# Kernel optimization log

Measured on AMD Instinct MI355X. Metric: run time of the kernel, lower is better.

## Reference

```python
import jax, jax.numpy as jnp
import numpy as np

WS = 16        # window size
NH = 8         # num heads
EPS = 1e-6
BN_EPS = 1e-5


def _l2norm(t):
    # normalize along the channel (d) axis, which is axis=-2, per position
    return t / jnp.linalg.norm(t, axis=-2, keepdims=True)


def setup_inputs() -> dict:
    key = jax.random.key(0)
    k1, k2, k3 = jax.random.split(key, 3)
    B, C, H, W = 8, 96, 256, 256
    x = jax.random.normal(k1, (B, C, H, W), dtype=jnp.float32)
    w_qkv = jax.random.normal(k2, (3 * C, C), dtype=jnp.float32) * (1.0 / np.sqrt(C))
    w_proj = jax.random.normal(k3, (C, C), dtype=jnp.float32) * (1.0 / np.sqrt(C))
    gamma = jnp.ones((C,), dtype=jnp.float32)
    beta = jnp.zeros((C,), dtype=jnp.float32)
    return {"x": x, "w_qkv": w_qkv, "w_proj": w_proj, "gamma": gamma, "beta": beta}


def reference(x, w_qkv, w_proj, gamma, beta):
    B, C, H, W = x.shape
    ws, nh = WS, NH
    d = C // nh
    # pad H, W up to multiples of ws (static shapes -> jit-safe)
    Hp = (H + ws - 1) // ws * ws
    Wp = (W + ws - 1) // ws * ws
    if (Hp, Wp) != (H, W):
        x = jnp.pad(x, ((0, 0), (0, 0), (0, Hp - H), (0, Wp - W)))
    hh, ww = Hp // ws, Wp // ws

    # 1x1 conv qkv projection (no bias)
    qkv = jnp.einsum('oc,bchw->bohw', w_qkv, x)  # [B, 3C, Hp, Wp]
    # rearrange 'b (qkv h d) (hh ws1) (ww ws2) -> qkv (b hh ww) h d (ws1 ws2)'
    qkv = qkv.reshape(B, 3, nh, d, hh, ws, ww, ws)
    qkv = qkv.transpose(1, 0, 4, 6, 2, 3, 5, 7).reshape(3, B * hh * ww, nh, d, ws * ws)
    q, k, v = qkv[0], qkv[1], qkv[2]  # each [bw, h, d, n]  (n = ws*ws)

    q = _l2norm(q).transpose(0, 1, 3, 2)  # [bw, h, n, d]
    k = _l2norm(k)                        # [bw, h, d, n]

    ksum = k.sum(axis=-1) + EPS           # [bw, h, d]
    tailor = 1.0 / (ws * ws + jnp.einsum('bhnc,bhc->bhn', q, ksum))  # [bw, h, n]

    kv = jnp.einsum('bhmn,bhcn->bhmc', k, v)     # [bw, h, d, d]
    attn = jnp.einsum('bhnm,bhmc->bhcn', q, kv)  # [bw, h, d, n]
    attn = attn + v.sum(axis=-1, keepdims=True)  # broadcast sum_n v over n
    attn = attn * tailor[:, :, None, :]

    # rearrange '(b hh ww) h d (ws1 ws2) -> b (h d) (hh ws1) (ww ws2)'
    out = attn.reshape(B, hh, ww, nh, d, ws, ws)
    out = out.transpose(0, 3, 4, 1, 5, 2, 6).reshape(B, C, Hp, Wp)
    out = out[:, :, :H, :W]

    # proj: 1x1 conv + BatchNorm2d (training-mode batch statistics)
    y = jnp.einsum('oc,bchw->bohw', w_proj, out)
    mean = y.mean(axis=(0, 2, 3), keepdims=True)
    var = y.var(axis=(0, 2, 3), keepdims=True)
    y = (y - mean) * jax.lax.rsqrt(var + BN_EPS)
    y = y * gamma[None, :, None, None] + beta[None, :, None, None]
    return y
```

## Files before the change

### kernel.cpp

```cpp
#include <hip/hip_runtime.h>

typedef short s8v __attribute__((ext_vector_type(8)));
typedef float f4v __attribute__((ext_vector_type(4)));

union F8 { int4 i; s8v s; };

__device__ __forceinline__ short f2bf(float f){
  union {float f; unsigned u;} v; v.f = f;
  unsigned r = (v.u + 0x7FFFu + ((v.u >> 16) & 1u)) >> 16;
  return (short)r;
}

#define MFMA(a,b,c) __builtin_amdgcn_mfma_f32_16x16x32_bf16((a),(b),(c),0,0,0)

#define WS_W2_OFF   58368
#define WS_ST_OFF   76800
#define WS_OUT_OFF  (1u<<20)

__global__ void prep_kernel(const float* __restrict__ wqkv, const float* __restrict__ wproj,
                            unsigned short* __restrict__ w1, unsigned short* __restrict__ w2,
                            float* __restrict__ stats){
  int i = blockIdx.x * 256 + threadIdx.x;
  for (int j = i; j < 304*96; j += gridDim.x * 256){
    int row = j / 96, c = j - row * 96;
    float v = (row < 288) ? wqkv[row * 96 + c] : 0.f;
    w1[j] = (unsigned short)f2bf(v);
  }
  for (int j = i; j < 96*96; j += gridDim.x * 256)
    w2[j] = (unsigned short)f2bf(wproj[j]);
  if (i < 192) stats[i] = 0.f;
}

__global__ __launch_bounds__(256) void attn_kernel(const float* __restrict__ x,
                                                   const unsigned short* __restrict__ w1,
                                                   float* __restrict__ outp){
  __shared__ short ks[16*264];
  __shared__ short vs[16*264];
  __shared__ short qsT[256*32];
  __shared__ short kvT[16*32];

  const int tid  = threadIdx.x;
  const int lane = tid & 63, wave = tid >> 6;
  const int quad = lane >> 4, col = lane & 15;
  const int wx = blockIdx.x, wy = blockIdx.y, b = blockIdx.z;
  const int h0 = wy * 16, w0 = wx * 16;

  for (int i = tid; i < 4*264; i += 256){
    int r = i / 264; int cc = i - r * 264; r += 12;
    short v = (r == 15) ? (short)0x3F80 : (short)0;
    ks[r*264 + cc] = v; vs[r*264 + cc] = v;
  }
  for (int i = tid; i < 256*32; i += 256){
    int m = i & 31;
    qsT[i] = (m == 12) ? (short)0x3F80 : (short)0;
  }
  for (int i = tid; i < 16*32; i += 256) kvT[i] = 0;

  const float* xb = x + ((size_t)b * 96 << 16);
  s8v Bf[4][3];
  #pragma unroll
  for (int jt = 0; jt < 4; ++jt){
    int t0 = wave * 64 + jt * 16;
    const float* px = xb + (size_t)(h0 + (t0 >> 4)) * 256 + (w0 + col);
    #pragma unroll
    for (int kt = 0; kt < 3; ++kt){
      F8 f;
      #pragma unroll
      for (int j = 0; j < 8; ++j){
        int c = kt * 32 + quad * 8 + j;
        f.s[j] = f2bf(px[(size_t)c << 16]);
      }
      Bf[jt][kt] = f.s;
    }
  }

  for (int h = 0; h < 8; ++h){
    s8v Af[3][3];
    #pragma unroll
    for (int mi = 0; mi < 3; ++mi){
      int row = mi * 96 + h * 12 + col;
      const unsigned short* pw = w1 + row * 96 + quad * 8;
      #pragma unroll
      for (int kt = 0; kt < 3; ++kt){
        F8 f; f.i = *(const int4*)(pw + kt * 32);
        Af[mi][kt] = f.s;
      }
    }
    f4v acc[3][4];
    #pragma unroll
    for (int mi = 0; mi < 3; ++mi)
      #pragma unroll
      for (int jt = 0; jt < 4; ++jt){
        f4v a = {0.f, 0.f, 0.f, 0.f};
        #pragma unroll
        for (int kt = 0; kt < 3; ++kt) a = MFMA(Af[mi][kt], Bf[jt][kt], a);
        acc[mi][jt] = a;
      }

    #pragma unroll
    for (int jt = 0; jt < 4; ++jt){
      int t = wave * 64 + jt * 16 + col;
      {
        f4v q = acc[0][jt];
        float s = (quad < 3) ? (q[0]*q[0] + q[1]*q[1] + q[2]*q[2] + q[3]*q[3]) : 0.f;
        s += __shfl_xor(s, 16, 64); s += __shfl_xor(s, 32, 64);
        float rq = rsqrtf(s);
        if (quad < 3){
          short4 pk; pk.x = f2bf(q[0]*rq); pk.y = f2bf(q[1]*rq); pk.z = f2bf(q[2]*rq); pk.w = f2bf(q[3]*rq);
          *(short4*)&qsT[t * 32 + quad * 4] = pk;
        }
      }
      {
        f4v k = acc[1][jt];
        float s = (quad < 3) ? (k[0]*k[0] + k[1]*k[1] + k[2]*k[2] + k[3]*k[3]) : 0.f;
        s += __shfl_xor(s, 16, 64); s += __shfl_xor(s, 32, 64);
        float rk = rsqrtf(s);
        f4v vv = acc[2][jt];
        if (quad < 3){
          #pragma unroll
          for (int r = 0; r < 4; ++r){
            ks[(quad*4 + r) * 264 + t] = f2bf(k[r] * rk);
            vs[(quad*4 + r) * 264 + t] = f2bf(vv[r]);
          }
        }
      }
    }
    __syncthreads();

    if (wave == 0){
      f4v kv = {0.f, 0.f, 0.f, 0.f};
      #pragma unroll
      for (int kk = 0; kk < 8; ++kk){
        F8 a, bb;
        a.i  = *(const int4*)&ks[col * 264 + kk * 32 + quad * 8];
        bb.i = *(const int4*)&vs[col * 264 + kk * 32 + quad * 8];
        kv = MFMA(a.s, bb.s, kv);
      }
      int c = col;
      if (c != 12){
        int row = (c == 15) ? 12 : c;
        if (quad < 3){
          short4 pk; pk.x = f2bf(kv[0]); pk.y = f2bf(kv[1]); pk.z = f2bf(kv[2]); pk.w = f2bf(kv[3]);
          *(short4*)&kvT[row * 32 + quad * 4] = pk;
        } else {
          short4 pk; pk.x = (c == 15) ? (short)0 : f2bf(kv[3]); pk.y = 0; pk.z = 0; pk.w = 0;
          *(short4*)&kvT[row * 32 + 12] = pk;
        }
      }
    }
    __syncthreads();

    {
      F8 af; af.i = *(const int4*)&kvT[col * 32 + quad * 8];
      #pragma unroll
      for (int jt = 0; jt < 4; ++jt){
        int t0 = wave * 64 + jt * 16;
        F8 bq; bq.i = *(const int4*)&qsT[(t0 + col) * 32 + quad * 8];
        f4v z = {0.f, 0.f, 0.f, 0.f};
        f4v d2 = MFMA(af.s, bq.s, z);
        float dot = __shfl(d2[0], 48 + col, 64);
        float tl = 1.f / (256.f + dot);
        if (quad < 3){
          float* po = outp + ((size_t)(b * 96 + h * 12 + quad * 4) << 16)
                      + (size_t)(h0 + (t0 >> 4)) * 256 + (w0 + col);
          #pragma unroll
          for (int r = 0; r < 4; ++r) po[(size_t)r << 16] = d2[r] * tl;
        }
      }
    }
    __syncthreads();
  }
}

__global__ __launch_bounds__(256) void proj_kernel(const float* __restrict__ outp,
                                                   const unsigned short* __restrict__ w2,
                                                   float* __restrict__ y,
                                                   float* __restrict__ stats){
  __shared__ float sld[192];
  const int tid = threadIdx.x;
  if (tid < 192) sld[tid] = 0.f;
  __syncthreads();
  const int lane = tid & 63, wave = tid >> 6;
  const int quad = lane >> 4, col = lane & 15;
  const int hrow = blockIdx.x, b = blockIdx.y;

  const float* ob = outp + ((size_t)b * 96 << 16) + (size_t)hrow * 256;
  s8v Bf[4][3];
  #pragma unroll
  for (int jt = 0; jt < 4; ++jt){
    int n0 = wave * 64 + jt * 16;
    const float* px = ob + n0 + col;
    #pragma unroll
    for (int kt = 0; kt < 3; ++kt){
      F8 f;
      #pragma unroll
      for (int j = 0; j < 8; ++j){
        int c = kt * 32 + quad * 8 + j;
        f.s[j] = f2bf(px[(size_t)c << 16]);
      }
      Bf[jt][kt] = f.s;
    }
  }
  float* yb = y + ((size_t)b * 96 << 16) + (size_t)hrow * 256;
  #pragma unroll
  for (int mt = 0; mt < 6; ++mt){
    s8v Af[3];
    #pragma unroll
    for (int kt = 0; kt < 3; ++kt){
      F8 f; f.i = *(const int4*)(w2 + (mt * 16 + col) * 96 + kt * 32 + quad * 8);
      Af[kt] = f.s;
    }
    float rs[4] = {0.f,0.f,0.f,0.f}, rss[4] = {0.f,0.f,0.f,0.f};
    #pragma unroll
    for (int jt = 0; jt < 4; ++jt){
      int n0 = wave * 64 + jt * 16;
      f4v a = {0.f, 0.f, 0.f, 0.f};
      #pragma unroll
      for (int kt = 0; kt < 3; ++kt) a = MFMA(Af[kt], Bf[jt][kt], a);
      float* pyo = yb + ((size_t)(mt * 16 + quad * 4) << 16) + n0 + col;
      #pragma unroll
      for (int r = 0; r < 4; ++r){
        float v = a[r];
        pyo[(size_t)r << 16] = v;
        rs[r] += v; rss[r] += v * v;
      }
    }
    #pragma unroll
    for (int r = 0; r < 4; ++r){
      float a1 = rs[r], a2 = rss[r];
      a1 += __shfl_xor(a1, 1, 64); a2 += __shfl_xor(a2, 1, 64);
      a1 += __shfl_xor(a1, 2, 64); a2 += __shfl_xor(a2, 2, 64);
      a1 += __shfl_xor(a1, 4, 64); a2 += __shfl_xor(a2, 4, 64);
      a1 += __shfl_xor(a1, 8, 64); a2 += __shfl_xor(a2, 8, 64);
      if (col == 0){
        int o = mt * 16 + quad * 4 + r;
        atomicAdd(&sld[o], a1);
        atomicAdd(&sld[96 + o], a2);
      }
    }
  }
  __syncthreads();
  if (tid < 192) atomicAdd(&stats[tid], sld[tid]);
}

__global__ __launch_bounds__(256) void bn_kernel(float* __restrict__ y,
                                                 const float* __restrict__ stats,
                                                 const float* __restrict__ gamma,
                                                 const float* __restrict__ beta){
  const int qq = blockIdx.x, c = blockIdx.y, b = blockIdx.z;
  const float invN = 1.f / 524288.f;
  float s = stats[c], ss = stats[96 + c];
  float mean = s * invN;
  float var  = ss * invN - mean * mean;
  float sc = gamma[c] * rsqrtf(var + 1e-5f);
  float sh = beta[c] - mean * sc;
  float4* p = (float4*)(y + ((size_t)(b * 96 + c) << 16) + (size_t)qq * 16384);
  int tid = threadIdx.x;
  #pragma unroll
  for (int i = 0; i < 16; ++i){
    float4 v = p[tid + i * 256];
    v.x = v.x * sc + sh; v.y = v.y * sc + sh; v.z = v.z * sc + sh; v.w = v.w * sc + sh;
    p[tid + i * 256] = v;
  }
}

extern "C" void kernel_launch(void* const* d_in, const int* in_sizes, int n_in,
                              void* d_out, int out_size, void* d_ws, size_t ws_size,
                              hipStream_t stream){
  const float* x     = (const float*)d_in[0];
  const float* wqkv  = (const float*)d_in[1];
  const float* wproj = (const float*)d_in[2];
  const float* gamma = (const float*)d_in[3];
  const float* beta  = (const float*)d_in[4];
  char* ws = (char*)d_ws;
  unsigned short* w1 = (unsigned short*)(ws);
  unsigned short* w2 = (unsigned short*)(ws + WS_W2_OFF);
  float* stats = (float*)(ws + WS_ST_OFF);
  float* outp  = (float*)(ws + WS_OUT_OFF);
  float* y = (float*)d_out;

  hipLaunchKernelGGL(prep_kernel, dim3(64), dim3(256), 0, stream, wqkv, wproj, w1, w2, stats);
  hipLaunchKernelGGL(attn_kernel, dim3(16, 16, 8), dim3(256), 0, stream, x, w1, outp);
  hipLaunchKernelGGL(proj_kernel, dim3(256, 8), dim3(256), 0, stream, outp, w2, y, stats);
  hipLaunchKernelGGL(bn_kernel, dim3(4, 96, 8), dim3(256), 0, stream, y, stats, gamma, beta);
}
```

Before: 613.4 us.

## Store attention output as bf16 channel-last and cut per-head syncs

The attention intermediate becomes bf16 in a pixel-major (channel-last) layout instead of fp32 channel-planar. This halves the intermediate traffic and lets the projection kernel load its operands as contiguous 16-byte vectors instead of strided scalar gathers plus conversion. The attention kernel double-buffers the k/v shared tiles and has every wave compute the kv product redundantly, building the transposed kv operand with lane shuffles, so two of the three barriers per head go away. The q, k and v projections are also computed one at a time to lower register pressure. The trade-offs are extra rounding on the intermediate, redundant MFMA work in every wave, and a tricky shuffle mapping that is easy to get wrong.

```diff
diff --git a/kernel.cpp b/kernel.cpp
--- a/kernel.cpp
+++ b/kernel.cpp
@@ -33,11 +33,10 @@
 
 __global__ __launch_bounds__(256) void attn_kernel(const float* __restrict__ x,
                                                    const unsigned short* __restrict__ w1,
-                                                   float* __restrict__ outp){
-  __shared__ short ks[16*264];
-  __shared__ short vs[16*264];
-  __shared__ short qsT[256*32];
-  __shared__ short kvT[16*32];
+                                                   short* __restrict__ outp){
+  __shared__ short ks[2][16*264];
+  __shared__ short vs[2][16*264];
+  __shared__ short qsT[256*40];
 
   const int tid  = threadIdx.x;
   const int lane = tid & 63, wave = tid >> 6;
@@ -45,16 +44,14 @@
   const int wx = blockIdx.x, wy = blockIdx.y, b = blockIdx.z;
   const int h0 = wy * 16, w0 = wx * 16;
 
-  for (int i = tid; i < 4*264; i += 256){
-    int r = i / 264; int cc = i - r * 264; r += 12;
+  for (int i = tid; i < 2*4*264; i += 256){
+    int buf = i / (4*264), j = i % (4*264);
+    int r = 12 + j / 264, cc = j % 264;
     short v = (r == 15) ? (short)0x3F80 : (short)0;
-    ks[r*264 + cc] = v; vs[r*264 + cc] = v;
-  }
-  for (int i = tid; i < 256*32; i += 256){
-    int m = i & 31;
-    qsT[i] = (m == 12) ? (short)0x3F80 : (short)0;
-  }
-  for (int i = tid; i < 16*32; i += 256) kvT[i] = 0;
+    ks[buf][r*264 + cc] = v; vs[buf][r*264 + cc] = v;
+  }
+  for (int i = tid; i < 256*40; i += 256)
+    qsT[i] = ((i % 40) == 12) ? (short)0x3F80 : (short)0;
 
   const float* xb = x + ((size_t)b * 96 << 16);
   s8v Bf[4][3];
@@ -75,104 +72,116 @@
   }
 
   for (int h = 0; h < 8; ++h){
-    s8v Af[3][3];
-    #pragma unroll
-    for (int mi = 0; mi < 3; ++mi){
-      int row = mi * 96 + h * 12 + col;
-      const unsigned short* pw = w1 + row * 96 + quad * 8;
+    const int p = h & 1;
+    {
+      s8v Aq[3];
       #pragma unroll
       for (int kt = 0; kt < 3; ++kt){
-        F8 f; f.i = *(const int4*)(pw + kt * 32);
-        Af[mi][kt] = f.s;
-      }
-    }
-    f4v acc[3][4];
-    #pragma unroll
-    for (int mi = 0; mi < 3; ++mi)
+        F8 f; f.i = *(const int4*)(w1 + (h*12 + col) * 96 + kt*32 + quad*8);
+        Aq[kt] = f.s;
+      }
       #pragma unroll
       for (int jt = 0; jt < 4; ++jt){
-        f4v a = {0.f, 0.f, 0.f, 0.f};
+        f4v a = {0.f,0.f,0.f,0.f};
         #pragma unroll
-        for (int kt = 0; kt < 3; ++kt) a = MFMA(Af[mi][kt], Bf[jt][kt], a);
-        acc[mi][jt] = a;
-      }
-
-    #pragma unroll
-    for (int jt = 0; jt < 4; ++jt){
-      int t = wave * 64 + jt * 16 + col;
-      {
-        f4v q = acc[0][jt];
-        float s = (quad < 3) ? (q[0]*q[0] + q[1]*q[1] + q[2]*q[2] + q[3]*q[3]) : 0.f;
+        for (int kt = 0; kt < 3; ++kt) a = MFMA(Aq[kt], Bf[jt][kt], a);
+        float s = (quad < 3) ? (a[0]*a[0] + a[1]*a[1] + a[2]*a[2] + a[3]*a[3]) : 0.f;
         s += __shfl_xor(s, 16, 64); s += __shfl_xor(s, 32, 64);
         float rq = rsqrtf(s);
         if (quad < 3){
-          short4 pk; pk.x = f2bf(q[0]*rq); pk.y = f2bf(q[1]*rq); pk.z = f2bf(q[2]*rq); pk.w = f2bf(q[3]*rq);
-          *(short4*)&qsT[t * 32 + quad * 4] = pk;
+          int t = wave*64 + jt*16 + col;
+          short4 pk; pk.x = f2bf(a[0]*rq); pk.y = f2bf(a[1]*rq); pk.z = f2bf(a[2]*rq); pk.w = f2bf(a[3]*rq);
+          *(short4*)&qsT[t*40 + quad*4] = pk;
         }
       }
-      {
-        f4v k = acc[1][jt];
-        float s = (quad < 3) ? (k[0]*k[0] + k[1]*k[1] + k[2]*k[2] + k[3]*k[3]) : 0.f;
+    }
+    {
+      s8v Ak[3];
+      #pragma unroll
+      for (int kt = 0; kt < 3; ++kt){
+        F8 f; f.i = *(const int4*)(w1 + (96 + h*12 + col) * 96 + kt*32 + quad*8);
+        Ak[kt] = f.s;
+      }
+      #pragma unroll
+      for (int jt = 0; jt < 4; ++jt){
+        f4v a = {0.f,0.f,0.f,0.f};
+        #pragma unroll
+        for (int kt = 0; kt < 3; ++kt) a = MFMA(Ak[kt], Bf[jt][kt], a);
+        float s = (quad < 3) ? (a[0]*a[0] + a[1]*a[1] + a[2]*a[2] + a[3]*a[3]) : 0.f;
         s += __shfl_xor(s, 16, 64); s += __shfl_xor(s, 32, 64);
         float rk = rsqrtf(s);
-        f4v vv = acc[2][jt];
         if (quad < 3){
+          int t = wave*64 + jt*16 + col;
           #pragma unroll
-          for (int r = 0; r < 4; ++r){
-            ks[(quad*4 + r) * 264 + t] = f2bf(k[r] * rk);
-            vs[(quad*4 + r) * 264 + t] = f2bf(vv[r]);
-          }
+          for (int r = 0; r < 4; ++r) ks[p][(quad*4 + r)*264 + t] = f2bf(a[r]*rk);
         }
       }
     }
+    {
+      s8v Av[3];
+      #pragma unroll
+      for (int kt = 0; kt < 3; ++kt){
+        F8 f; f.i = *(const int4*)(w1 + (192 + h*12 + col) * 96 + kt*32 + quad*8);
+        Av[kt] = f.s;
+      }
+      #pragma unroll
+      for (int jt = 0; jt < 4; ++jt){
+        f4v a = {0.f,0.f,0.f,0.f};
+        #pragma unroll
+        for (int kt = 0; kt < 3; ++kt) a = MFMA(Av[kt], Bf[jt][kt], a);
+        if (quad < 3){
+          int t = wave*64 + jt*16 + col;
+          #pragma unroll
+          for (int r = 0; r < 4; ++r) vs[p][(quad*4 + r)*264 + t] = f2bf(a[r]);
+        }
+      }
+    }
     __syncthreads();
 
-    if (wave == 0){
-      f4v kv = {0.f, 0.f, 0.f, 0.f};
-      #pragma unroll
-      for (int kk = 0; kk < 8; ++kk){
-        F8 a, bb;
-        a.i  = *(const int4*)&ks[col * 264 + kk * 32 + quad * 8];
-        bb.i = *(const int4*)&vs[col * 264 + kk * 32 + quad * 8];
-        kv = MFMA(a.s, bb.s, kv);
-      }
-      int c = col;
-      if (c != 12){
-        int row = (c == 15) ? 12 : c;
-        if (quad < 3){
-          short4 pk; pk.x = f2bf(kv[0]); pk.y = f2bf(kv[1]); pk.z = f2bf(kv[2]); pk.w = f2bf(kv[3]);
-          *(short4*)&kvT[row * 32 + quad * 4] = pk;
-        } else {
-          short4 pk; pk.x = (c == 15) ? (short)0 : f2bf(kv[3]); pk.y = 0; pk.z = 0; pk.w = 0;
-          *(short4*)&kvT[row * 32 + 12] = pk;
-        }
-      }
-    }
-    __syncthreads();
-
-    {
-      F8 af; af.i = *(const int4*)&kvT[col * 32 + quad * 8];
-      #pragma unroll
-      for (int jt = 0; jt < 4; ++jt){
-        int t0 = wave * 64 + jt * 16;
-        F8 bq; bq.i = *(const int4*)&qsT[(t0 + col) * 32 + quad * 8];
-        f4v z = {0.f, 0.f, 0.f, 0.f};
-        f4v d2 = MFMA(af.s, bq.s, z);
-        float dot = __shfl(d2[0], 48 + col, 64);
-        float tl = 1.f / (256.f + dot);
-        if (quad < 3){
-          float* po = outp + ((size_t)(b * 96 + h * 12 + quad * 4) << 16)
-                      + (size_t)(h0 + (t0 >> 4)) * 256 + (w0 + col);
-          #pragma unroll
-          for (int r = 0; r < 4; ++r) po[(size_t)r << 16] = d2[r] * tl;
-        }
-      }
-    }
-    __syncthreads();
-  }
-}
-
-__global__ __launch_bounds__(256) void proj_kernel(const float* __restrict__ outp,
+    f4v kvv = {0.f,0.f,0.f,0.f};
+    #pragma unroll
+    for (int kk = 0; kk < 8; ++kk){
+      F8 a, bv;
+      a.i  = *(const int4*)&ks[p][col*264 + kk*32 + quad*8];
+      bv.i = *(const int4*)&vs[p][col*264 + kk*32 + quad*8];
+      kvv = MFMA(a.s, bv.s, kvv);
+    }
+    F8 fa;
+    {
+      int cc = (col == 12) ? 15 : col;
+      int l0 = ((quad << 1) << 4) | cc;
+      int l1 = (((quad << 1) + 1) << 4) | cc;
+      float v;
+      v = __shfl(kvv[0], l0 & 63, 64); fa.s[0] = f2bf((quad < 2) ? v : 0.f);
+      v = __shfl(kvv[1], l0 & 63, 64); fa.s[1] = f2bf((quad < 2) ? v : 0.f);
+      v = __shfl(kvv[2], l0 & 63, 64); fa.s[2] = f2bf((quad < 2) ? v : 0.f);
+      v = __shfl(kvv[3], l0 & 63, 64); fa.s[3] = f2bf((quad < 2) ? v : 0.f);
+      float v0  = __shfl(kvv[0], l1 & 63, 64);
+      float v15 = __shfl(kvv[3], 48 | cc, 64);
+      fa.s[4] = f2bf((quad == 0) ? v0 : ((quad == 1) ? v15 : 0.f));
+      v = __shfl(kvv[1], l1 & 63, 64); fa.s[5] = f2bf((quad == 0) ? v : 0.f);
+      v = __shfl(kvv[2], l1 & 63, 64); fa.s[6] = f2bf((quad == 0) ? v : 0.f);
+      v = __shfl(kvv[3], l1 & 63, 64); fa.s[7] = f2bf((quad == 0) ? v : 0.f);
+    }
+    #pragma unroll
+    for (int jt = 0; jt < 4; ++jt){
+      int t0 = wave*64 + jt*16;
+      F8 bq; bq.i = *(const int4*)&qsT[(t0 + col)*40 + quad*8];
+      f4v z = {0.f,0.f,0.f,0.f};
+      f4v d2 = MFMA(fa.s, bq.s, z);
+      float dot = __shfl(d2[0], 48 + col, 64);
+      float tl = 1.f / dot;
+      if (quad < 3){
+        int pix = (h0 + (t0 >> 4)) * 256 + (w0 + col);
+        short* po = outp + ((size_t)(b << 16) + pix) * 96 + h*12 + quad*4;
+        short4 pk; pk.x = f2bf(d2[0]*tl); pk.y = f2bf(d2[1]*tl); pk.z = f2bf(d2[2]*tl); pk.w = f2bf(d2[3]*tl);
+        *(short4*)po = pk;
+      }
+    }
+  }
+}
+
+__global__ __launch_bounds__(256) void proj_kernel(const short* __restrict__ outp,
                                                    const unsigned short* __restrict__ w2,
                                                    float* __restrict__ y,
                                                    float* __restrict__ stats){
@@ -184,40 +193,35 @@
   const int quad = lane >> 4, col = lane & 15;
   const int hrow = blockIdx.x, b = blockIdx.y;
 
-  const float* ob = outp + ((size_t)b * 96 << 16) + (size_t)hrow * 256;
+  const size_t pixbase = (size_t)(b << 16) + (size_t)hrow * 256;
   s8v Bf[4][3];
   #pragma unroll
   for (int jt = 0; jt < 4; ++jt){
-    int n0 = wave * 64 + jt * 16;
-    const float* px = ob + n0 + col;
+    int n0 = wave*64 + jt*16;
+    const short* pb = outp + (pixbase + n0 + col) * 96 + quad*8;
     #pragma unroll
     for (int kt = 0; kt < 3; ++kt){
-      F8 f;
-      #pragma unroll
-      for (int j = 0; j < 8; ++j){
-        int c = kt * 32 + quad * 8 + j;
-        f.s[j] = f2bf(px[(size_t)c << 16]);
-      }
+      F8 f; f.i = *(const int4*)(pb + kt*32);
       Bf[jt][kt] = f.s;
     }
   }
-  float* yb = y + ((size_t)b * 96 << 16) + (size_t)hrow * 256;
+  float* yb = y + ((size_t)(b*96) << 16) + (size_t)hrow * 256;
   #pragma unroll
   for (int mt = 0; mt < 6; ++mt){
     s8v Af[3];
     #pragma unroll
     for (int kt = 0; kt < 3; ++kt){
-      F8 f; f.i = *(const int4*)(w2 + (mt * 16 + col) * 96 + kt * 32 + quad * 8);
+      F8 f; f.i = *(const int4*)(w2 + (mt*16 + col)*96 + kt*32 + quad*8);
       Af[kt] = f.s;
     }
     float rs[4] = {0.f,0.f,0.f,0.f}, rss[4] = {0.f,0.f,0.f,0.f};
     #pragma unroll
     for (int jt = 0; jt < 4; ++jt){
-      int n0 = wave * 64 + jt * 16;
-      f4v a = {0.f, 0.f, 0.f, 0.f};
+      int n0 = wave*64 + jt*16;
+      f4v a = {0.f,0.f,0.f,0.f};
       #pragma unroll
       for (int kt = 0; kt < 3; ++kt) a = MFMA(Af[kt], Bf[jt][kt], a);
-      float* pyo = yb + ((size_t)(mt * 16 + quad * 4) << 16) + n0 + col;
+      float* pyo = yb + ((size_t)(mt*16 + quad*4) << 16) + n0 + col;
       #pragma unroll
       for (int r = 0; r < 4; ++r){
         float v = a[r];
@@ -233,7 +237,7 @@
       a1 += __shfl_xor(a1, 4, 64); a2 += __shfl_xor(a2, 4, 64);
       a1 += __shfl_xor(a1, 8, 64); a2 += __shfl_xor(a2, 8, 64);
       if (col == 0){
-        int o = mt * 16 + quad * 4 + r;
+        int o = mt*16 + quad*4 + r;
         atomicAdd(&sld[o], a1);
         atomicAdd(&sld[96 + o], a2);
       }
@@ -276,7 +280,7 @@
   unsigned short* w1 = (unsigned short*)(ws);
   unsigned short* w2 = (unsigned short*)(ws + WS_W2_OFF);
   float* stats = (float*)(ws + WS_ST_OFF);
-  float* outp  = (float*)(ws + WS_OUT_OFF);
+  short* outp  = (short*)(ws + WS_OUT_OFF);
   float* y = (float*)d_out;
 
   hipLaunchKernelGGL(prep_kernel, dim3(64), dim3(256), 0, stream, wqkv, wproj, w1, w2, stats);
```

Result: no change. 606.9 us (-1.1%).
